# Performance work log

Hardware: AMD Instinct MI355X
Metric: run time of the kernel (lower is better)

The kernel has to match this reference:

```python
import jax, jax.numpy as jnp
import numpy as np

B, N, H = 4, 256, 512
P = 128  # game_physics_params


def _init(key, shape, scale=0.02):
    return jax.random.normal(key, shape, dtype=jnp.float32) * scale


def setup_inputs() -> dict:
    key = jax.random.key(0)
    ks = jax.random.split(key, 16)
    return {
        "object_features": jax.random.normal(ks[0], (B, N, H), dtype=jnp.float32),
        # physics_predictor: H -> 512 -> P
        "pp_w1": _init(ks[1], (H, 512)), "pp_b1": jnp.zeros((512,), jnp.float32),
        "pp_w2": _init(ks[2], (512, P)), "pp_b2": jnp.zeros((P,), jnp.float32),
        # collision_detector: 2H -> 256 -> 128 -> 1
        "cd_w1": _init(ks[3], (2 * H, 256)), "cd_b1": jnp.zeros((256,), jnp.float32),
        "cd_w2": _init(ks[4], (256, 128)), "cd_b2": jnp.zeros((128,), jnp.float32),
        "cd_w3": _init(ks[5], (128, 1)), "cd_b3": jnp.zeros((1,), jnp.float32),
        # velocity / force heads: H -> 3
        "vel_w": _init(ks[6], (H, 3)), "vel_b": jnp.zeros((3,), jnp.float32),
        "frc_w": _init(ks[7], (H, 3)), "frc_b": jnp.zeros((3,), jnp.float32),
    }


def reference(object_features, pp_w1, pp_b1, pp_w2, pp_b2,
              cd_w1, cd_b1, cd_w2, cd_b2, cd_w3, cd_b3,
              vel_w, vel_b, frc_w, frc_b):
    x = object_features  # [B, N, H]
    # physics predictor MLP
    p = jax.nn.relu(x @ pp_w1 + pp_b1) @ pp_w2 + pp_b2  # [B, N, P]
    mass = jax.nn.sigmoid(p[..., 0:1]) * 100.0
    friction = jax.nn.sigmoid(p[..., 1:2])
    elasticity = jax.nn.sigmoid(p[..., 2:3])
    density = jax.nn.sigmoid(p[..., 3:4]) * 10.0
    velocities = x @ vel_w + vel_b  # [B, N, 3]
    forces = x @ frc_w + frc_b      # [B, N, 3]

    # vectorized pairwise collision detection over upper-triangle pairs
    iu, ju = np.triu_indices(N, k=1)  # static index arrays, length Np = N(N-1)/2
    pairs = jnp.concatenate([x[:, iu], x[:, ju]], axis=-1)  # [B, Np, 2H]
    h = jax.nn.relu(pairs @ cd_w1 + cd_b1)
    h = jax.nn.relu(h @ cd_w2 + cd_b2)
    prob = jax.nn.sigmoid(h @ cd_w3 + cd_b3)[..., 0]  # [B, Np]
    collision_matrix = jnp.zeros((x.shape[0], N, N), dtype=x.dtype)
    collision_matrix = collision_matrix.at[:, iu, ju].set(prob).at[:, ju, iu].set(prob)

    return (mass, friction, elasticity, density, velocities, forces, collision_matrix)
```

## Files before the change

### kernel.cpp

```cpp
#include <hip/hip_runtime.h>
#include <hip/hip_bf16.h>

typedef __attribute__((ext_vector_type(8))) short bf16x8;
typedef __attribute__((ext_vector_type(4))) float f32x4;

__device__ __forceinline__ float sigmoidf_(float v) {
    return 1.0f / (1.0f + __expf(-v));
}
__device__ __forceinline__ short f2bf(float f) {
    union { __hip_bfloat16 h; short s; } cv;
    cv.h = __float2bfloat16(f);
    return cv.s;
}
__device__ __forceinline__ float bf2f(short s) {
    union { float f; unsigned u; } cv;
    cv.u = ((unsigned)(unsigned short)s) << 16;
    return cv.f;
}

__global__ __launch_bounds__(256) void convert_kernel(
    const float* __restrict__ x, const float* __restrict__ pp_w1,
    const float* __restrict__ cd_w1, const float* __restrict__ cd_w2,
    const float* __restrict__ pp_w2, const float* __restrict__ vel_w,
    const float* __restrict__ frc_w,
    __hip_bfloat16* __restrict__ xb, __hip_bfloat16* __restrict__ Wt,
    __hip_bfloat16* __restrict__ w2t, float* __restrict__ hw)
{
    __shared__ float ts[64][65];
    const int b = blockIdx.x, t = threadIdx.x;

    if (b < 256) {
        int base = b * 2048 + t * 8;
        float4 a = *(const float4*)(x + base);
        float4 c = *(const float4*)(x + base + 4);
        bf16x8 o;
        o[0] = f2bf(a.x); o[1] = f2bf(a.y); o[2] = f2bf(a.z); o[3] = f2bf(a.w);
        o[4] = f2bf(c.x); o[5] = f2bf(c.y); o[6] = f2bf(c.z); o[7] = f2bf(c.w);
        *(bf16x8*)(xb + base) = o;
        return;
    }
    if (b == 392) {
        for (int e = t; e < 5120; e += 256) {
            int h = e >> 9, k = e & 511;
            float v = (h < 4) ? pp_w2[k * 128 + h]
                    : (h < 7) ? vel_w[k * 3 + (h - 4)]
                              : frc_w[k * 3 + (h - 7)];
            hw[e] = v;
        }
        return;
    }

    const float* src; int ss, k0, n0, region;
    if (b < 320)      { int i = b - 256; src = pp_w1; ss = 512; k0 = (i >> 3) * 64; n0 = (i & 7) * 64; region = 0; }
    else if (b < 384) { int i = b - 320; src = cd_w1; ss = 256; k0 = (i >> 2) * 64; n0 = (i & 3) * 64; region = 1; }
    else              { int i = b - 384; src = cd_w2; ss = 128; k0 = (i >> 1) * 64; n0 = (i & 1) * 64; region = 2; }

    #pragma unroll
    for (int i = 0; i < 4; ++i) {
        int r = (t >> 4) + i * 16, c4 = (t & 15) * 4;
        *(float4*)&ts[r][c4] = *(const float4*)(src + (k0 + r) * ss + n0 + c4);
    }
    __syncthreads();
    #pragma unroll
    for (int i = 0; i < 4; ++i) {
        int nOut = (t >> 4) + i * 16, kc = (t & 15) * 4;
        ushort4 o;
        o.x = (unsigned short)f2bf(ts[kc + 0][nOut]);
        o.y = (unsigned short)f2bf(ts[kc + 1][nOut]);
        o.z = (unsigned short)f2bf(ts[kc + 2][nOut]);
        o.w = (unsigned short)f2bf(ts[kc + 3][nOut]);
        int gn = n0 + nOut, gk = k0 + kc;
        if (region == 0)      *(ushort4*)(Wt + gn * 512 + gk) = o;
        else if (region == 1) {
            int row = (gk < 512) ? (512 + gn) : (768 + gn);
            *(ushort4*)(Wt + row * 512 + (gk & 511)) = o;
        } else                *(ushort4*)(w2t + gn * 256 + gk) = o;
    }
}

__global__ __launch_bounds__(256) void gemm_kernel(
    const __hip_bfloat16* __restrict__ xb, const __hip_bfloat16* __restrict__ Wt,
    const float* __restrict__ pp_b1, const float* __restrict__ cd_b1,
    __hip_bfloat16* __restrict__ hidg, __hip_bfloat16* __restrict__ Ugb,
    __hip_bfloat16* __restrict__ Vgb)
{
    const int t = threadIdx.x;
    const int wave = t >> 6, lane = t & 63;
    const int l = lane & 15, q = lane >> 4;
    const int m0 = blockIdx.y * 32;
    const int n0 = blockIdx.x * 128 + wave * 32;

    const __hip_bfloat16* a0p = xb + (m0 + l) * 512 + q * 8;
    const __hip_bfloat16* a1p = a0p + 16 * 512;
    const __hip_bfloat16* b0p = Wt + (n0 + l) * 512 + q * 8;
    const __hip_bfloat16* b1p = b0p + 16 * 512;

    f32x4 acc00 = {}, acc01 = {}, acc10 = {}, acc11 = {};
    #pragma unroll
    for (int ks = 0; ks < 16; ++ks) {
        bf16x8 a0 = *(const bf16x8*)(a0p + ks * 32);
        bf16x8 a1 = *(const bf16x8*)(a1p + ks * 32);
        bf16x8 b0 = *(const bf16x8*)(b0p + ks * 32);
        bf16x8 b1 = *(const bf16x8*)(b1p + ks * 32);
        acc00 = __builtin_amdgcn_mfma_f32_16x16x32_bf16(a0, b0, acc00, 0, 0, 0);
        acc01 = __builtin_amdgcn_mfma_f32_16x16x32_bf16(a0, b1, acc01, 0, 0, 0);
        acc10 = __builtin_amdgcn_mfma_f32_16x16x32_bf16(a1, b0, acc10, 0, 0, 0);
        acc11 = __builtin_amdgcn_mfma_f32_16x16x32_bf16(a1, b1, acc11, 0, 0, 0);
    }

    const int c0 = n0 + l, c1 = n0 + 16 + l;
    #pragma unroll
    for (int mt = 0; mt < 2; ++mt) {
        const f32x4& A0 = mt ? acc10 : acc00;
        const f32x4& A1 = mt ? acc11 : acc01;
        if (n0 < 512) {
            float b0v = pp_b1[c0], b1v = pp_b1[c1];
            #pragma unroll
            for (int r = 0; r < 4; ++r) {
                int rg = m0 + mt * 16 + q * 4 + r;
                hidg[rg * 512 + c0] = __float2bfloat16(fmaxf(A0[r] + b0v, 0.f));
                hidg[rg * 512 + c1] = __float2bfloat16(fmaxf(A1[r] + b1v, 0.f));
            }
        } else if (n0 < 768) {
            float b0v = cd_b1[c0 - 512], b1v = cd_b1[c1 - 512];
            #pragma unroll
            for (int r = 0; r < 4; ++r) {
                int rg = m0 + mt * 16 + q * 4 + r;
                Ugb[rg * 256 + (c0 - 512)] = __float2bfloat16(A0[r] + b0v);
                Ugb[rg * 256 + (c1 - 512)] = __float2bfloat16(A1[r] + b1v);
            }
        } else {
            #pragma unroll
            for (int r = 0; r < 4; ++r) {
                int rg = m0 + mt * 16 + q * 4 + r;
                Vgb[rg * 256 + (c0 - 768)] = __float2bfloat16(A0[r]);
                Vgb[rg * 256 + (c1 - 768)] = __float2bfloat16(A1[r]);
            }
        }
    }
}

__global__ __launch_bounds__(256, 2) void pair_kernel(
    const __hip_bfloat16* __restrict__ Ugb, const __hip_bfloat16* __restrict__ Vgb,
    const __hip_bfloat16* __restrict__ w2t,
    const float* __restrict__ cd_b2, const float* __restrict__ cd_w3,
    const float* __restrict__ cd_b3, float* __restrict__ cm,
    const float* __restrict__ x, const __hip_bfloat16* __restrict__ hidg,
    const float* __restrict__ hw, const float* __restrict__ pp_b2,
    const float* __restrict__ vel_b, const float* __restrict__ frc_b,
    float* __restrict__ out)
{
    __shared__ __align__(16) char smem[52224];

    const int t = threadIdx.x;
    const int wave = t >> 6, lane = t & 63;
    const int bx = blockIdx.x;

    if (bx >= 528) {
        float* hwl = (float*)smem;
        #pragma unroll
        for (int i = 0; i < 5; ++i) {
            int idx = i * 256 + t;
            ((float4*)hwl)[idx] = ((const float4*)hw)[idx];
        }
        __syncthreads();

        const int row0 = (bx - 528) * 8 + wave * 2;
        const float4* xr0 = (const float4*)(x + row0 * 512);
        const float4* xr1 = (const float4*)(x + (row0 + 1) * 512);
        float4 xa0 = xr0[lane * 2], xc0 = xr0[lane * 2 + 1];
        float4 xa1 = xr1[lane * 2], xc1 = xr1[lane * 2 + 1];
        bf16x8 hb0 = *(const bf16x8*)(hidg + row0 * 512 + lane * 8);
        bf16x8 hb1 = *(const bf16x8*)(hidg + (row0 + 1) * 512 + lane * 8);

        #pragma unroll
        for (int rr = 0; rr < 2; ++rr) {
            const int row = row0 + rr;
            float4 xa = rr ? xa1 : xa0, xc = rr ? xc1 : xc0;
            bf16x8 hb = rr ? hb1 : hb0;
            float hf[8];
            #pragma unroll
            for (int j = 0; j < 8; ++j) hf[j] = bf2f(hb[j]);

            #pragma unroll
            for (int h = 0; h < 10; ++h) {
                const float4* wr = (const float4*)(hwl + h * 512);
                float4 wa = wr[lane * 2], wc = wr[lane * 2 + 1];
                float s;
                if (h < 4) {
                    s = hf[0]*wa.x + hf[1]*wa.y + hf[2]*wa.z + hf[3]*wa.w
                      + hf[4]*wc.x + hf[5]*wc.y + hf[6]*wc.z + hf[7]*wc.w;
                } else {
                    s = xa.x*wa.x + xa.y*wa.y + xa.z*wa.z + xa.w*wa.w
                      + xc.x*wc.x + xc.y*wc.y + xc.z*wc.z + xc.w*wc.w;
                }
                s += __shfl_xor(s, 1);  s += __shfl_xor(s, 2);
                s += __shfl_xor(s, 4);  s += __shfl_xor(s, 8);
                s += __shfl_xor(s, 16); s += __shfl_xor(s, 32);
                if (lane == 0) {
                    if (h < 4) {
                        float sg = sigmoidf_(s + pp_b2[h]);
                        out[h * 1024 + row] = (h == 0) ? sg * 100.f : (h == 3) ? sg * 10.f : sg;
                    } else if (h < 7) {
                        out[4096 + row * 3 + (h - 4)] = s + vel_b[h - 4];
                    } else {
                        out[7168 + row * 3 + (h - 7)] = s + frc_b[h - 7];
                    }
                }
            }
        }
        return;
    }

    char* rawBB = smem;
    char* hsB   = smem + 32768;
    float (*ps)[64][4] = (float (*)[64][4])(smem + 32768 + 17408);

    const int tp = bx;
    int ti = (int)((65.0f - sqrtf(4225.0f - 8.0f * (float)tp)) * 0.5f);
    while ((ti + 1) * (65 - (ti + 1)) / 2 <= tp) ++ti;
    while (ti * (65 - ti) / 2 > tp) --ti;
    const int tj = ti + (tp - ti * (65 - ti) / 2);
    const int i0 = ti * 8, j0 = tj * 8;

    const int l = lane & 15, q = lane >> 4;

    const __hip_bfloat16* wb0 = w2t + ((wave * 2 + 0) * 16 + l) * 256 + q * 8;
    const __hip_bfloat16* wb1 = wb0 + 16 * 256;
    bf16x8 w2r0[8], w2r1[8];
    #pragma unroll
    for (int ks = 0; ks < 8; ++ks) {
        w2r0[ks] = *(const bf16x8*)(wb0 + ks * 32);
        w2r1[ks] = *(const bf16x8*)(wb1 + ks * 32);
    }
    const float b2v0 = cd_b2[(wave * 2 + 0) * 16 + l];
    const float b2v1 = cd_b2[(wave * 2 + 1) * 16 + l];
    const float w3v0 = cd_w3[(wave * 2 + 0) * 16 + l];
    const float w3v1 = cd_w3[(wave * 2 + 1) * 16 + l];
    const float b3 = cd_b3[0];

    __builtin_amdgcn_sched_barrier(0);
    {
        const int r0 = wave * 2;
        const int rlane = r0 + (lane >> 5);
        const int slot = lane & 31;
        #pragma unroll
        for (int u = 0; u < 4; ++u) {
            const int gk16 = slot ^ (rlane & 7);
            const __hip_bfloat16* us = Ugb + ((u << 8) + i0 + rlane) * 256 + gk16 * 8;
            const __hip_bfloat16* vs = Vgb + ((u << 8) + j0 + rlane) * 256 + gk16 * 8;
            char* du = rawBB + (((u << 1) + 0) * 8 + r0) * 512;
            char* dv = rawBB + (((u << 1) + 1) * 8 + r0) * 512;
            __builtin_amdgcn_global_load_lds(
                (const __attribute__((address_space(1))) void*)us,
                (__attribute__((address_space(3))) void*)du, 16, 0, 0);
            __builtin_amdgcn_global_load_lds(
                (const __attribute__((address_space(1))) void*)vs,
                (__attribute__((address_space(3))) void*)dv, 16, 0, 0);
        }
    }
    __builtin_amdgcn_sched_barrier(0);

    f32x4 acc[4][2];

    auto CVT = [&](int u, int h) {
        const char* RU = rawBB + ((u << 1) + 0) * 4096;
        const char* RV = rawBB + ((u << 1) + 1) * 4096;
        const int ur = lane >> 3, vr = lane & 7;
        #pragma unroll
        for (int i = 0; i < 4; ++i) {
            const int s16 = (wave << 2) + i;
            const int gs = (h << 4) + s16;
            bf16x8 ub = *(const bf16x8*)(RU + ur * 512 + ((gs ^ ur) << 4));
            bf16x8 vb = *(const bf16x8*)(RV + vr * 512 + ((gs ^ vr) << 4));
            bf16x8 o;
            #pragma unroll
            for (int j = 0; j < 8; ++j)
                o[j] = f2bf(fmaxf(bf2f(ub[j]) + bf2f(vb[j]), 0.f));
            *(bf16x8*)(hsB + s16 * 1088 + lane * 16) = o;
        }
    };
    auto MFMAH = [&](int h) {
        #pragma unroll
        for (int ks = 0; ks < 4; ++ks) {
            bf16x8 bfr0 = w2r0[h * 4 + ks];
            bf16x8 bfr1 = w2r1[h * 4 + ks];
            #pragma unroll
            for (int mt = 0; mt < 4; ++mt) {
                bf16x8 afr = *(const bf16x8*)(hsB + (ks * 4 + q) * 1088 + (mt * 16 + l) * 16);
                acc[mt][0] = __builtin_amdgcn_mfma_f32_16x16x32_bf16(afr, bfr0, acc[mt][0], 0, 0, 0);
                acc[mt][1] = __builtin_amdgcn_mfma_f32_16x16x32_bf16(afr, bfr1, acc[mt][1], 0, 0, 0);
            }
        }
    };
    auto EPI = [&](int u) {
        #pragma unroll
        for (int mt = 0; mt < 4; ++mt) {
            #pragma unroll
            for (int r = 0; r < 4; ++r) {
                float g0 = fmaxf(acc[mt][0][r] + b2v0, 0.f);
                float g1 = fmaxf(acc[mt][1][r] + b2v1, 0.f);
                float s = g0 * w3v0 + g1 * w3v1;
                s += __shfl_xor(s, 1);
                s += __shfl_xor(s, 2);
                s += __shfl_xor(s, 4);
                s += __shfl_xor(s, 8);
                if (l == 0) ps[u & 1][mt * 16 + q * 4 + r][wave] = s;
            }
        }
    };
    auto FIN = [&](int u) {
        if (t < 64) {
            int p = t;
            float v = ps[u & 1][p][0] + ps[u & 1][p][1] + ps[u & 1][p][2]
                    + ps[u & 1][p][3] + b3;
            float prob = 1.0f / (1.0f + __expf(-v));
            int i = i0 + (p >> 3), j = j0 + (p & 7);
            float* base = cm + u * 65536;
            if (i < j) {
                base[i * 256 + j] = prob;
                base[j * 256 + i] = prob;
            } else if (i == j) {
                base[i * 256 + i] = 0.0f;
            }
        }
    };

    #pragma unroll
    for (int u = 0; u < 4; ++u) {
        if (u == 0)      asm volatile("s_waitcnt vmcnt(6) lgkmcnt(0)" ::: "memory");
        else if (u == 1) asm volatile("s_waitcnt vmcnt(4) lgkmcnt(0)" ::: "memory");
        else if (u == 2) asm volatile("s_waitcnt vmcnt(2) lgkmcnt(0)" ::: "memory");
        else             asm volatile("s_waitcnt vmcnt(0) lgkmcnt(0)" ::: "memory");
        __builtin_amdgcn_s_barrier();
        __builtin_amdgcn_sched_barrier(0);

        #pragma unroll
        for (int mt = 0; mt < 4; ++mt) {
            acc[mt][0] = (f32x4){0.f, 0.f, 0.f, 0.f};
            acc[mt][1] = (f32x4){0.f, 0.f, 0.f, 0.f};
        }

        CVT(u, 0);
        if (u >= 1) FIN(u - 1);
        asm volatile("s_waitcnt lgkmcnt(0)" ::: "memory");
        __builtin_amdgcn_s_barrier();
        __builtin_amdgcn_sched_barrier(0);

        MFMAH(0);
        __builtin_amdgcn_s_barrier();
        __builtin_amdgcn_sched_barrier(0);

        CVT(u, 1);
        asm volatile("s_waitcnt lgkmcnt(0)" ::: "memory");
        __builtin_amdgcn_s_barrier();
        __builtin_amdgcn_sched_barrier(0);

        MFMAH(1);
        EPI(u);
    }
    asm volatile("s_waitcnt lgkmcnt(0)" ::: "memory");
    __builtin_amdgcn_s_barrier();
    FIN(3);
}

extern "C" void kernel_launch(void* const* d_in, const int* in_sizes, int n_in,
                              void* d_out, int out_size, void* d_ws, size_t ws_size,
                              hipStream_t stream) {
    const float* x     = (const float*)d_in[0];
    const float* pp_w1 = (const float*)d_in[1];
    const float* pp_b1 = (const float*)d_in[2];
    const float* pp_w2 = (const float*)d_in[3];
    const float* pp_b2 = (const float*)d_in[4];
    const float* cd_w1 = (const float*)d_in[5];
    const float* cd_b1 = (const float*)d_in[6];
    const float* cd_w2 = (const float*)d_in[7];
    const float* cd_b2 = (const float*)d_in[8];
    const float* cd_w3 = (const float*)d_in[9];
    const float* cd_b3 = (const float*)d_in[10];
    const float* vel_w = (const float*)d_in[11];
    const float* vel_b = (const float*)d_in[12];
    const float* frc_w = (const float*)d_in[13];
    const float* frc_b = (const float*)d_in[14];

    float* out = (float*)d_out;
    __hip_bfloat16* Ugb  = (__hip_bfloat16*)d_ws;
    __hip_bfloat16* Vgb  = Ugb + 262144;
    __hip_bfloat16* xb   = Vgb + 262144;
    __hip_bfloat16* Wt   = xb + 524288;
    __hip_bfloat16* hidg = Wt + 524288;
    __hip_bfloat16* w2t  = hidg + 524288;
    float* hw = (float*)(w2t + 32768);

    convert_kernel<<<dim3(393), dim3(256), 0, stream>>>(
        x, pp_w1, cd_w1, cd_w2, pp_w2, vel_w, frc_w, xb, Wt, w2t, hw);
    gemm_kernel<<<dim3(8, 32), dim3(256), 0, stream>>>(
        xb, Wt, pp_b1, cd_b1, hidg, Ugb, Vgb);
    pair_kernel<<<dim3(656), dim3(256), 0, stream>>>(
        Ugb, Vgb, w2t, cd_b2, cd_w3, cd_b3, out + 10240,
        x, hidg, hw, pp_b2, vel_b, frc_b, out);
}
```

Before: 126.7 us.

## Split pair kernel tiles across batch halves to double block count

Each pair tile block now handles two of the four batches instead of all four, so the grid grows from 528 to 1056 pair blocks and LDS per block shrinks from about 52KB to 35KB. The aim is to fill the GPU better and allow more resident blocks per CU. The cost is that every block reloads the w2 weight fragments into registers, so that load work doubles. Those weight loads are also rewritten as inline asm global_load_dwordx4 between sched barriers, which fixes their issue order relative to the vmcnt waits.

```diff
diff --git a/kernel.cpp b/kernel.cpp
--- a/kernel.cpp
+++ b/kernel.cpp
@@ -150,13 +150,13 @@
     const float* __restrict__ vel_b, const float* __restrict__ frc_b,
     float* __restrict__ out)
 {
-    __shared__ __align__(16) char smem[52224];
+    __shared__ __align__(16) char smem[35840];
 
     const int t = threadIdx.x;
     const int wave = t >> 6, lane = t & 63;
     const int bx = blockIdx.x;
 
-    if (bx >= 528) {
+    if (bx >= 1056) {
         float* hwl = (float*)smem;
         #pragma unroll
         for (int i = 0; i < 5; ++i) {
@@ -165,7 +165,7 @@
         }
         __syncthreads();
 
-        const int row0 = (bx - 528) * 8 + wave * 2;
+        const int row0 = (bx - 1056) * 8 + wave * 2;
         const float4* xr0 = (const float4*)(x + row0 * 512);
         const float4* xr1 = (const float4*)(x + (row0 + 1) * 512);
         float4 xa0 = xr0[lane * 2], xc0 = xr0[lane * 2 + 1];
@@ -213,10 +213,11 @@
     }
 
     char* rawBB = smem;
-    char* hsB   = smem + 32768;
-    float (*ps)[64][4] = (float (*)[64][4])(smem + 32768 + 17408);
-
-    const int tp = bx;
+    char* hsB   = smem + 16384;
+    float (*ps)[64][4] = (float (*)[64][4])(smem + 16384 + 17408);
+
+    const int tp = bx >> 1;
+    const int ub = (bx & 1) << 1;
     int ti = (int)((65.0f - sqrtf(4225.0f - 8.0f * (float)tp)) * 0.5f);
     while ((ti + 1) * (65 - (ti + 1)) / 2 <= tp) ++ti;
     while (ti * (65 - ti) / 2 > tp) --ti;
@@ -228,11 +229,16 @@
     const __hip_bfloat16* wb0 = w2t + ((wave * 2 + 0) * 16 + l) * 256 + q * 8;
     const __hip_bfloat16* wb1 = wb0 + 16 * 256;
     bf16x8 w2r0[8], w2r1[8];
+    __builtin_amdgcn_sched_barrier(0);
     #pragma unroll
     for (int ks = 0; ks < 8; ++ks) {
-        w2r0[ks] = *(const bf16x8*)(wb0 + ks * 32);
-        w2r1[ks] = *(const bf16x8*)(wb1 + ks * 32);
-    }
+        asm volatile("global_load_dwordx4 %0, %1, off"
+                     : "=&v"(w2r0[ks]) : "v"(wb0 + ks * 32));
+        asm volatile("global_load_dwordx4 %0, %1, off"
+                     : "=&v"(w2r1[ks]) : "v"(wb1 + ks * 32));
+    }
+    __builtin_amdgcn_sched_barrier(0);
+
     const float b2v0 = cd_b2[(wave * 2 + 0) * 16 + l];
     const float b2v1 = cd_b2[(wave * 2 + 1) * 16 + l];
     const float w3v0 = cd_w3[(wave * 2 + 0) * 16 + l];
@@ -244,13 +250,14 @@
         const int r0 = wave * 2;
         const int rlane = r0 + (lane >> 5);
         const int slot = lane & 31;
-        #pragma unroll
-        for (int u = 0; u < 4; ++u) {
-            const int gk16 = slot ^ (rlane & 7);
+        const int gk16 = slot ^ (rlane & 7);
+        #pragma unroll
+        for (int ul = 0; ul < 2; ++ul) {
+            const int u = ub + ul;
             const __hip_bfloat16* us = Ugb + ((u << 8) + i0 + rlane) * 256 + gk16 * 8;
             const __hip_bfloat16* vs = Vgb + ((u << 8) + j0 + rlane) * 256 + gk16 * 8;
-            char* du = rawBB + (((u << 1) + 0) * 8 + r0) * 512;
-            char* dv = rawBB + (((u << 1) + 1) * 8 + r0) * 512;
+            char* du = rawBB + (((ul << 1) + 0) * 8 + r0) * 512;
+            char* dv = rawBB + (((ul << 1) + 1) * 8 + r0) * 512;
             __builtin_amdgcn_global_load_lds(
                 (const __attribute__((address_space(1))) void*)us,
                 (__attribute__((address_space(3))) void*)du, 16, 0, 0);
@@ -263,20 +270,20 @@
 
     f32x4 acc[4][2];
 
-    auto CVT = [&](int u, int h) {
-        const char* RU = rawBB + ((u << 1) + 0) * 4096;
-        const char* RV = rawBB + ((u << 1) + 1) * 4096;
-        const int ur = lane >> 3, vr = lane & 7;
+    const int ur = lane >> 3, vr = lane & 7;
+    auto CVT = [&](int ul, int h) {
+        const char* RU = rawBB + ((ul << 1) + 0) * 4096;
+        const char* RV = rawBB + ((ul << 1) + 1) * 4096;
         #pragma unroll
         for (int i = 0; i < 4; ++i) {
             const int s16 = (wave << 2) + i;
             const int gs = (h << 4) + s16;
-            bf16x8 ub = *(const bf16x8*)(RU + ur * 512 + ((gs ^ ur) << 4));
-            bf16x8 vb = *(const bf16x8*)(RV + vr * 512 + ((gs ^ vr) << 4));
+            bf16x8 ubv = *(const bf16x8*)(RU + ur * 512 + ((gs ^ ur) << 4));
+            bf16x8 vbv = *(const bf16x8*)(RV + vr * 512 + ((gs ^ vr) << 4));
             bf16x8 o;
             #pragma unroll
             for (int j = 0; j < 8; ++j)
-                o[j] = f2bf(fmaxf(bf2f(ub[j]) + bf2f(vb[j]), 0.f));
+                o[j] = f2bf(fmaxf(bf2f(ubv[j]) + bf2f(vbv[j]), 0.f));
             *(bf16x8*)(hsB + s16 * 1088 + lane * 16) = o;
         }
     };
@@ -327,11 +334,9 @@
     };
 
     #pragma unroll
-    for (int u = 0; u < 4; ++u) {
-        if (u == 0)      asm volatile("s_waitcnt vmcnt(6) lgkmcnt(0)" ::: "memory");
-        else if (u == 1) asm volatile("s_waitcnt vmcnt(4) lgkmcnt(0)" ::: "memory");
-        else if (u == 2) asm volatile("s_waitcnt vmcnt(2) lgkmcnt(0)" ::: "memory");
-        else             asm volatile("s_waitcnt vmcnt(0) lgkmcnt(0)" ::: "memory");
+    for (int ul = 0; ul < 2; ++ul) {
+        if (ul == 0) asm volatile("s_waitcnt vmcnt(2) lgkmcnt(0)" ::: "memory");
+        else         asm volatile("s_waitcnt vmcnt(0) lgkmcnt(0)" ::: "memory");
         __builtin_amdgcn_s_barrier();
         __builtin_amdgcn_sched_barrier(0);
 
@@ -341,8 +346,8 @@
             acc[mt][1] = (f32x4){0.f, 0.f, 0.f, 0.f};
         }
 
-        CVT(u, 0);
-        if (u >= 1) FIN(u - 1);
+        CVT(ul, 0);
+        if (ul == 1) FIN(ub);
         asm volatile("s_waitcnt lgkmcnt(0)" ::: "memory");
         __builtin_amdgcn_s_barrier();
         __builtin_amdgcn_sched_barrier(0);
@@ -351,17 +356,17 @@
         __builtin_amdgcn_s_barrier();
         __builtin_amdgcn_sched_barrier(0);
 
-        CVT(u, 1);
+        CVT(ul, 1);
         asm volatile("s_waitcnt lgkmcnt(0)" ::: "memory");
         __builtin_amdgcn_s_barrier();
         __builtin_amdgcn_sched_barrier(0);
 
         MFMAH(1);
-        EPI(u);
+        EPI(ub + ul);
     }
     asm volatile("s_waitcnt lgkmcnt(0)" ::: "memory");
     __builtin_amdgcn_s_barrier();
-    FIN(3);
+    FIN(ub + 1);
 }
 
 extern "C" void kernel_launch(void* const* d_in, const int* in_sizes, int n_in,
@@ -396,7 +401,7 @@
         x, pp_w1, cd_w1, cd_w2, pp_w2, vel_w, frc_w, xb, Wt, w2t, hw);
     gemm_kernel<<<dim3(8, 32), dim3(256), 0, stream>>>(
         xb, Wt, pp_b1, cd_b1, hidg, Ugb, Vgb);
-    pair_kernel<<<dim3(656), dim3(256), 0, stream>>>(
+    pair_kernel<<<dim3(1184), dim3(256), 0, stream>>>(
         Ugb, Vgb, w2t, cd_b2, cd_w3, cd_b3, out + 10240,
         x, hidg, hw, pp_b2, vel_b, frc_b, out);
 }
```

Measured after the change: 133.6 us. 1.05x slower.
